# Kernel tuning notes

Measured on AMD Instinct MI355X. Metric: run time of the kernel, lower is better.

## Reference

```python
import jax, jax.numpy as jnp
import numpy as np

N_NODES = 100000
N_EDGES = 1000000
D_IN = 64
D_HID = 64
D_OUT = 64
LL_OUT = 16
NUM_REL = 5
METAPATH = (0, 1, 2)


def setup_inputs() -> dict:
    key = jax.random.key(0)
    ks = jax.random.split(key, 12)
    s = 0.05  # small init scale
    x = jax.random.normal(ks[0], (N_NODES, D_IN), dtype=jnp.float32)
    edge_index = jax.random.randint(ks[1], (2, N_EDGES), 0, N_NODES, dtype=jnp.int64)
    edge_type = jax.random.randint(ks[2], (N_EDGES,), 0, NUM_REL, dtype=jnp.int64)
    # conv1: per-relation weights + root weight + bias (input_dim -> hidden_dim)
    W1 = jax.random.normal(ks[3], (NUM_REL, D_IN, D_HID), dtype=jnp.float32) * s
    root1 = jax.random.normal(ks[4], (D_IN, D_HID), dtype=jnp.float32) * s
    b1 = jnp.zeros((D_HID,), dtype=jnp.float32)
    # conv2: hidden_dim -> output_dim (reused for all layers > 0)
    W2 = jax.random.normal(ks[5], (NUM_REL, D_HID, D_OUT), dtype=jnp.float32) * s
    root2 = jax.random.normal(ks[6], (D_HID, D_OUT), dtype=jnp.float32) * s
    b2 = jnp.zeros((D_OUT,), dtype=jnp.float32)
    # final linear layer (output_dim -> ll_output_dim)
    Wl = jax.random.normal(ks[7], (D_OUT, LL_OUT), dtype=jnp.float32) * s
    bl = jnp.zeros((LL_OUT,), dtype=jnp.float32)
    return {
        "x": x, "edge_index": edge_index, "edge_type": edge_type,
        "W1": W1, "root1": root1, "b1": b1,
        "W2": W2, "root2": root2, "b2": b2,
        "Wl": Wl, "bl": bl,
    }


def _rgcn_single_rel(rel, x, src, dst, edge_type, W, root, b):
    """RGCN conv restricted to one relation `rel`.

    flow='target_to_source': messages are gathered from the target node
    (edge_index[1]) and aggregated (sum) at the source node (edge_index[0]).
    Edges of other relation types are masked out (jit-friendly equivalent
    of boolean edge filtering).
    """
    mask = (edge_type == rel).astype(x.dtype)[:, None]          # [E, 1]
    msg = (x[dst] * mask) @ W[rel]                              # [E, d_out]
    agg = jax.ops.segment_sum(msg, src, num_segments=N_NODES)   # [N, d_out]
    return agg + x @ root + b


def reference(x, edge_index, edge_type, W1, root1, b1, W2, root2, b2, Wl, bl):
    src, dst = edge_index[0], edge_index[1]
    for layer_index, rel in enumerate(METAPATH):
        if layer_index == 0:
            x = jax.nn.relu(_rgcn_single_rel(rel, x, src, dst, edge_type, W1, root1, b1))
        else:
            x = jax.nn.relu(_rgcn_single_rel(rel, x, src, dst, edge_type, W2, root2, b2))
    logits = x @ Wl + bl
    return jax.nn.log_softmax(logits, axis=1)
```

## Files before the change

### kernel.cpp

```cpp
#include <hip/hip_runtime.h>
#include <hip/hip_bf16.h>
#include <math.h>

#define N_NODES 100000
#define N_EDGES 1000000
#define D 64
#define N3 300000
#define BCAP 16
#define BM 128
#define AST 72
#define BST 72
#define GEMM_BLOCKS ((N_NODES + BM - 1) / BM)
#define FILL_BLOCKS ((N_EDGES + 1023) / 1024)

typedef __attribute__((ext_vector_type(8))) short bf16x8;
typedef __attribute__((ext_vector_type(4))) float f32x4;

static __device__ __forceinline__ float bf2f(unsigned short u) {
    union { unsigned int i; float f; } c; c.i = ((unsigned int)u) << 16; return c.f;
}
static __device__ __forceinline__ float lo16(unsigned int u) { return bf2f((unsigned short)(u & 0xffffu)); }
static __device__ __forceinline__ float hi16(unsigned int u) { return bf2f((unsigned short)(u >> 16)); }
static __device__ __forceinline__ unsigned short f2bf(float f) {
    union { float f; unsigned int i; } c; c.f = f;
    unsigned int i = c.i;
    return (unsigned short)((i + 0x7FFFu + ((i >> 16) & 1u)) >> 16);
}
static __device__ __forceinline__ unsigned int pk2(float lo, float hi) {
    return (unsigned int)f2bf(lo) | ((unsigned int)f2bf(hi) << 16);
}

static __device__ __forceinline__ void fill_body4(
    const int* __restrict__ src, const int* __restrict__ dst,
    const int* __restrict__ et, int* __restrict__ cnt, int* __restrict__ bucket,
    int e0)
{
    if (e0 >= N_EDGES) return;
    int4 t4 = *(const int4*)(et + e0);
    int4 s4 = *(const int4*)(src + e0);
    int4 d4 = *(const int4*)(dst + e0);
    int t[4] = { t4.x, t4.y, t4.z, t4.w };
    int s[4] = { s4.x, s4.y, s4.z, s4.w };
    int d[4] = { d4.x, d4.y, d4.z, d4.w };
#pragma unroll
    for (int i = 0; i < 4; ++i) {
        if (t[i] < 3) {
            int base = t[i] * N_NODES + s[i];
            int pos = atomicAdd(&cnt[base], 1);
            if (pos < BCAP) bucket[(size_t)base * BCAP + pos] = d[i];
        }
    }
}

static __device__ __forceinline__ void gemm_body(
    int bid,
    const float* __restrict__ Hin, const unsigned short* __restrict__ Pp,
    const unsigned short* __restrict__ Yp,
    const int* __restrict__ cnt, const int* __restrict__ bucket, int relG,
    const float* __restrict__ Wm, const float* __restrict__ Rm,
    const float* __restrict__ bias,
    unsigned short* __restrict__ Y16, unsigned short* __restrict__ P16, int nN)
{
    __shared__ unsigned short At[BM][AST];
    __shared__ unsigned short Bt[128][BST];
    int t = threadIdx.x;
    int n0 = bid * BM;

#pragma unroll
    for (int it = 0; it < 8; ++it) {
        int idx = t + it * 256;
        int col = idx & 127;
        int k0  = (idx >> 7) * 4;
        const float* srcB = (col < 64) ? (Wm + col) : (Rm + col - 64);
        ushort4 wv;
        wv.x = f2bf(srcB[(k0 + 0) * 64]);
        wv.y = f2bf(srcB[(k0 + 1) * 64]);
        wv.z = f2bf(srcB[(k0 + 2) * 64]);
        wv.w = f2bf(srcB[(k0 + 3) * 64]);
        *(ushort4*)&Bt[col][k0] = wv;
    }

    {
        int gidx = t >> 4, j = t & 15, lane = t & 63, grp = lane & 48;
        if (relG < 0) {
#pragma unroll
            for (int pass = 0; pass < 8; ++pass) {
                int rw = gidx + pass * 16;
                int node = n0 + rw;
                float4 v = make_float4(0.f, 0.f, 0.f, 0.f);
                if (node < nN) v = *(const float4*)(Hin + (size_t)node * 64 + j * 4);
                ushort4 av;
                av.x = f2bf(v.x); av.y = f2bf(v.y); av.z = f2bf(v.z); av.w = f2bf(v.w);
                *(ushort4*)&At[rw][j * 4] = av;
            }
        } else {
            int nn[8]; int bk[8]; ushort4 pv[8];
#pragma unroll
            for (int p = 0; p < 8; ++p) {
                int node = n0 + gidx + p * 16;
                int nodeC = (node < nN) ? node : 0;
                int base = relG * N_NODES + nodeC;
                nn[p] = cnt[base];
                bk[p] = bucket[(size_t)base * BCAP + j];
                pv[p] = *(const ushort4*)(Pp + (size_t)nodeC * 64 + j * 4);
            }
#pragma unroll
            for (int p = 0; p < 8; ++p) {
                int rw = gidx + p * 16;
                int node = n0 + rw;
                float4 v = make_float4(0.f, 0.f, 0.f, 0.f);
                if (node < nN) {
                    v = make_float4(bf2f(pv[p].x), bf2f(pv[p].y),
                                    bf2f(pv[p].z), bf2f(pv[p].w));
                    int n = nn[p]; if (n > BCAP) n = BCAP;
                    for (int k = 0; k < n; k += 4) {
                        int i1 = (k + 1 < n) ? k + 1 : k;
                        int i2 = (k + 2 < n) ? k + 2 : k;
                        int i3 = (k + 3 < n) ? k + 3 : k;
                        int dn0 = __shfl(bk[p], grp | k);
                        int dn1 = __shfl(bk[p], grp | i1);
                        int dn2 = __shfl(bk[p], grp | i2);
                        int dn3 = __shfl(bk[p], grp | i3);
                        ushort4 u0 = *(const ushort4*)(Yp + (size_t)dn0 * 64 + j * 4);
                        ushort4 u1 = *(const ushort4*)(Yp + (size_t)dn1 * 64 + j * 4);
                        ushort4 u2 = *(const ushort4*)(Yp + (size_t)dn2 * 64 + j * 4);
                        ushort4 u3 = *(const ushort4*)(Yp + (size_t)dn3 * 64 + j * 4);
                        v.x += bf2f(u0.x); v.y += bf2f(u0.y);
                        v.z += bf2f(u0.z); v.w += bf2f(u0.w);
                        if (k + 1 < n) {
                            v.x += bf2f(u1.x); v.y += bf2f(u1.y);
                            v.z += bf2f(u1.z); v.w += bf2f(u1.w);
                        }
                        if (k + 2 < n) {
                            v.x += bf2f(u2.x); v.y += bf2f(u2.y);
                            v.z += bf2f(u2.z); v.w += bf2f(u2.w);
                        }
                        if (k + 3 < n) {
                            v.x += bf2f(u3.x); v.y += bf2f(u3.y);
                            v.z += bf2f(u3.z); v.w += bf2f(u3.w);
                        }
                    }
                    v.x = fmaxf(v.x, 0.f); v.y = fmaxf(v.y, 0.f);
                    v.z = fmaxf(v.z, 0.f); v.w = fmaxf(v.w, 0.f);
                }
                ushort4 av;
                av.x = f2bf(v.x); av.y = f2bf(v.y); av.z = f2bf(v.z); av.w = f2bf(v.w);
                *(ushort4*)&At[rw][j * 4] = av;
            }
        }
    }
    __syncthreads();

    int w  = t >> 6;
    int l  = t & 63;
    int ln = l & 15;
    int lk = l >> 4;
    f32x4 acc[2][8];
#pragma unroll
    for (int nt = 0; nt < 2; ++nt)
#pragma unroll
        for (int ct = 0; ct < 8; ++ct)
            acc[nt][ct] = (f32x4){0.f, 0.f, 0.f, 0.f};

    bf16x8 af[2][2];
#pragma unroll
    for (int nt = 0; nt < 2; ++nt)
#pragma unroll
        for (int ks = 0; ks < 2; ++ks)
            af[nt][ks] = *(const bf16x8*)&At[w * 32 + nt * 16 + ln][ks * 32 + lk * 8];

#pragma unroll
    for (int ct = 0; ct < 8; ++ct) {
        bf16x8 bf0 = *(const bf16x8*)&Bt[ct * 16 + ln][lk * 8];
        bf16x8 bf1 = *(const bf16x8*)&Bt[ct * 16 + ln][32 + lk * 8];
#pragma unroll
        for (int nt = 0; nt < 2; ++nt) {
            acc[nt][ct] = __builtin_amdgcn_mfma_f32_16x16x32_bf16(bf0, af[nt][0], acc[nt][ct], 0, 0, 0);
            acc[nt][ct] = __builtin_amdgcn_mfma_f32_16x16x32_bf16(bf1, af[nt][1], acc[nt][ct], 0, 0, 0);
        }
    }

#pragma unroll
    for (int ct = 0; ct < 8; ++ct) {
        int c0 = ct * 16 + lk * 4;
#pragma unroll
        for (int nt = 0; nt < 2; ++nt) {
            int node = n0 + w * 32 + nt * 16 + ln;
            if (node >= nN) continue;
            f32x4 v = acc[nt][ct];
            if (ct < 4) {
                uint2 u;
                u.x = pk2(v[0], v[1]);
                u.y = pk2(v[2], v[3]);
                *(uint2*)(Y16 + (size_t)node * 64 + c0) = u;
            } else {
                const float4 bv = *(const float4*)(bias + (c0 - 64));
                uint2 u;
                u.x = pk2(v[0] + bv.x, v[1] + bv.y);
                u.y = pk2(v[2] + bv.z, v[3] + bv.w);
                *(uint2*)(P16 + (size_t)node * 64 + (c0 - 64)) = u;
            }
        }
    }
}

__global__ __launch_bounds__(256) void fused0_kernel(
    const float* __restrict__ x,
    const int* __restrict__ src, const int* __restrict__ dst,
    const int* __restrict__ et, int* __restrict__ cnt, int* __restrict__ bucket,
    const float* __restrict__ Wm, const float* __restrict__ Rm,
    const float* __restrict__ bias,
    unsigned short* __restrict__ Y16, unsigned short* __restrict__ P16, int nN)
{
    if (blockIdx.x < GEMM_BLOCKS) {
        gemm_body(blockIdx.x, x, nullptr, nullptr, nullptr, nullptr, -1,
                  Wm, Rm, bias, Y16, P16, nN);
    } else {
        int e0 = ((blockIdx.x - GEMM_BLOCKS) * 256 + threadIdx.x) * 4;
        fill_body4(src, dst, et, cnt, bucket, e0);
    }
}

__global__ __launch_bounds__(256) void gemm_node_kernel(
    const unsigned short* __restrict__ Pp, const unsigned short* __restrict__ Yp,
    const int* __restrict__ cnt, const int* __restrict__ bucket, int rel,
    const float* __restrict__ Wm, const float* __restrict__ Rm,
    const float* __restrict__ bias,
    unsigned short* __restrict__ Y16, unsigned short* __restrict__ P16, int nN)
{
    gemm_body(blockIdx.x, nullptr, Pp, Yp, cnt, bucket, rel,
              Wm, Rm, bias, Y16, P16, nN);
}

__global__ __launch_bounds__(256) void final_kernel(
    const unsigned short* __restrict__ P2, const unsigned short* __restrict__ Y2,
    const int* __restrict__ cnt, const int* __restrict__ bucket, int rel,
    const float* __restrict__ Wl, const float* __restrict__ bl,
    float* __restrict__ out, int nN)
{
    int t = threadIdx.x;
    int w = t >> 6, l = t & 63;
    int ln = l & 15, lk = l >> 4;
    int node = blockIdx.x * 64 + w * 16 + ln;

    bf16x8 wf[2];
#pragma unroll
    for (int ks = 0; ks < 2; ++ks) {
        union { bf16x8 v; unsigned short u[8]; } tmp;
#pragma unroll
        for (int i = 0; i < 8; ++i)
            tmp.u[i] = f2bf(Wl[(ks * 32 + lk * 8 + i) * 16 + ln]);
        wf[ks] = tmp.v;
    }

    float v[16];
#pragma unroll
    for (int i = 0; i < 16; ++i) v[i] = 0.f;
    if (node < nN) {
#pragma unroll
        for (int ks = 0; ks < 2; ++ks) {
            uint4 pu = *(const uint4*)(P2 + (size_t)node * 64 + ks * 32 + lk * 8);
            v[ks * 8 + 0] = lo16(pu.x); v[ks * 8 + 1] = hi16(pu.x);
            v[ks * 8 + 2] = lo16(pu.y); v[ks * 8 + 3] = hi16(pu.y);
            v[ks * 8 + 4] = lo16(pu.z); v[ks * 8 + 5] = hi16(pu.z);
            v[ks * 8 + 6] = lo16(pu.w); v[ks * 8 + 7] = hi16(pu.w);
        }
        int base = rel * N_NODES + node;
        int n = cnt[base]; if (n > BCAP) n = BCAP;
        const int* brow = bucket + (size_t)base * BCAP;
        for (int k = 0; k < n; k += 2) {
            int dn0 = brow[k];
            int dn1 = (k + 1 < n) ? brow[k + 1] : dn0;
            uint4 a0 = *(const uint4*)(Y2 + (size_t)dn0 * 64 + lk * 8);
            uint4 a1 = *(const uint4*)(Y2 + (size_t)dn0 * 64 + 32 + lk * 8);
            uint4 b0 = *(const uint4*)(Y2 + (size_t)dn1 * 64 + lk * 8);
            uint4 b1 = *(const uint4*)(Y2 + (size_t)dn1 * 64 + 32 + lk * 8);
            v[0] += lo16(a0.x); v[1] += hi16(a0.x);
            v[2] += lo16(a0.y); v[3] += hi16(a0.y);
            v[4] += lo16(a0.z); v[5] += hi16(a0.z);
            v[6] += lo16(a0.w); v[7] += hi16(a0.w);
            v[8]  += lo16(a1.x); v[9]  += hi16(a1.x);
            v[10] += lo16(a1.y); v[11] += hi16(a1.y);
            v[12] += lo16(a1.z); v[13] += hi16(a1.z);
            v[14] += lo16(a1.w); v[15] += hi16(a1.w);
            if (k + 1 < n) {
                v[0] += lo16(b0.x); v[1] += hi16(b0.x);
                v[2] += lo16(b0.y); v[3] += hi16(b0.y);
                v[4] += lo16(b0.z); v[5] += hi16(b0.z);
                v[6] += lo16(b0.w); v[7] += hi16(b0.w);
                v[8]  += lo16(b1.x); v[9]  += hi16(b1.x);
                v[10] += lo16(b1.y); v[11] += hi16(b1.y);
                v[12] += lo16(b1.z); v[13] += hi16(b1.z);
                v[14] += lo16(b1.w); v[15] += hi16(b1.w);
            }
        }
#pragma unroll
        for (int i = 0; i < 16; ++i) v[i] = fmaxf(v[i], 0.f);
    }
    union { bf16x8 bv; unsigned short u[8]; } af[2];
#pragma unroll
    for (int ks = 0; ks < 2; ++ks)
#pragma unroll
        for (int i = 0; i < 8; ++i) af[ks].u[i] = f2bf(v[ks * 8 + i]);

    f32x4 acc = (f32x4){0.f, 0.f, 0.f, 0.f};
    acc = __builtin_amdgcn_mfma_f32_16x16x32_bf16(wf[0], af[0].bv, acc, 0, 0, 0);
    acc = __builtin_amdgcn_mfma_f32_16x16x32_bf16(wf[1], af[1].bv, acc, 0, 0, 0);

    if (node < nN) {
        float4 blv = *(const float4*)(bl + lk * 4);
        float p0 = acc[0] + blv.x, p1 = acc[1] + blv.y;
        float p2 = acc[2] + blv.z, p3 = acc[3] + blv.w;
        float mx = fmaxf(fmaxf(p0, p1), fmaxf(p2, p3));
        mx = fmaxf(mx, __shfl_xor(mx, 16));
        mx = fmaxf(mx, __shfl_xor(mx, 32));
        float s = __expf(p0 - mx) + __expf(p1 - mx) + __expf(p2 - mx) + __expf(p3 - mx);
        s += __shfl_xor(s, 16);
        s += __shfl_xor(s, 32);
        float ls = logf(s) + mx;
        float4 r = make_float4(p0 - ls, p1 - ls, p2 - ls, p3 - ls);
        *(float4*)(out + (size_t)node * 16 + lk * 4) = r;
    }
}

extern "C" void kernel_launch(void* const* d_in, const int* in_sizes, int n_in,
                              void* d_out, int out_size, void* d_ws, size_t ws_size,
                              hipStream_t stream) {
    const float* x     = (const float*)d_in[0];
    const int*   ei    = (const int*)  d_in[1];
    const int*   et    = (const int*)  d_in[2];
    const float* W1    = (const float*)d_in[3];
    const float* root1 = (const float*)d_in[4];
    const float* b1    = (const float*)d_in[5];
    const float* W2    = (const float*)d_in[6];
    const float* root2 = (const float*)d_in[7];
    const float* b2    = (const float*)d_in[8];
    const float* Wl    = (const float*)d_in[9];
    const float* bl    = (const float*)d_in[10];
    float* out = (float*)d_out;

    const int N = N_NODES, E = N_EDGES;
    const size_t hBytes   = (size_t)N * D * sizeof(unsigned short);
    const size_t cntBytes = ((size_t)N3 * sizeof(int) + 255) & ~(size_t)255;
    const size_t bktBytes = ((size_t)N3 * BCAP * sizeof(int) + 255) & ~(size_t)255;

    char* ws = (char*)d_ws;
    unsigned short* Ya = (unsigned short*)ws;                 ws += hBytes;
    unsigned short* Yb = (unsigned short*)ws;                 ws += hBytes;
    unsigned short* Pa = (unsigned short*)ws;                 ws += hBytes;
    unsigned short* Pb = (unsigned short*)ws;                 ws += hBytes;
    int* cnt    = (int*)ws;                                   ws += cntBytes;
    int* bucket = (int*)ws;                                   ws += bktBytes;

    const int* src = ei;
    const int* dst = ei + E;

    const int finalBlocks = (N + 63) / 64;

    hipMemsetAsync(cnt, 0, (size_t)N3 * sizeof(int), stream);

    fused0_kernel<<<GEMM_BLOCKS + FILL_BLOCKS, 256, 0, stream>>>(
        x, src, dst, et, cnt, bucket, W1 + 0 * D * D, root1, b1, Ya, Pa, N);

    gemm_node_kernel<<<GEMM_BLOCKS, 256, 0, stream>>>(
        Pa, Ya, cnt, bucket, 0, W2 + 1 * D * D, root2, b2, Yb, Pb, N);

    gemm_node_kernel<<<GEMM_BLOCKS, 256, 0, stream>>>(
        Pb, Yb, cnt, bucket, 1, W2 + 2 * D * D, root2, b2, Ya, Pa, N);

    final_kernel<<<finalBlocks, 256, 0, stream>>>(
        Pa, Ya, cnt, bucket, 2, Wl, bl, out, N);
}
```

Measured before the change: 108.5 us.

## Split per-relation bucket fill across layer kernels to overlap with GEMMs

The edge bucketing for relations 1 and 2 is no longer done entirely in the first fused kernel. Each kernel now fills only the relation needed by the next layer, in extra blocks that run alongside the current layer's GEMM blocks. This spreads the atomic-heavy fill work across three launches so it can overlap with compute instead of all sitting in the first launch. In exchange, the edge arrays are read three times instead of once, and each later kernel gets more blocks.

```diff
diff --git a/kernel.cpp b/kernel.cpp
--- a/kernel.cpp
+++ b/kernel.cpp
@@ -33,7 +33,7 @@
 static __device__ __forceinline__ void fill_body4(
     const int* __restrict__ src, const int* __restrict__ dst,
     const int* __restrict__ et, int* __restrict__ cnt, int* __restrict__ bucket,
-    int e0)
+    int e0, int rel)
 {
     if (e0 >= N_EDGES) return;
     int4 t4 = *(const int4*)(et + e0);
@@ -44,8 +44,8 @@
     int d[4] = { d4.x, d4.y, d4.z, d4.w };
 #pragma unroll
     for (int i = 0; i < 4; ++i) {
-        if (t[i] < 3) {
-            int base = t[i] * N_NODES + s[i];
+        if (t[i] == rel) {
+            int base = rel * N_NODES + s[i];
             int pos = atomicAdd(&cnt[base], 1);
             if (pos < BCAP) bucket[(size_t)base * BCAP + pos] = d[i];
         }
@@ -217,19 +217,26 @@
                   Wm, Rm, bias, Y16, P16, nN);
     } else {
         int e0 = ((blockIdx.x - GEMM_BLOCKS) * 256 + threadIdx.x) * 4;
-        fill_body4(src, dst, et, cnt, bucket, e0);
-    }
-}
-
-__global__ __launch_bounds__(256) void gemm_node_kernel(
+        fill_body4(src, dst, et, cnt, bucket, e0, 0);
+    }
+}
+
+__global__ __launch_bounds__(256) void gemm_fill_kernel(
     const unsigned short* __restrict__ Pp, const unsigned short* __restrict__ Yp,
-    const int* __restrict__ cnt, const int* __restrict__ bucket, int rel,
+    const int* __restrict__ src, const int* __restrict__ dst,
+    const int* __restrict__ et, int* __restrict__ cnt, int* __restrict__ bucket,
+    int relG, int relF,
     const float* __restrict__ Wm, const float* __restrict__ Rm,
     const float* __restrict__ bias,
     unsigned short* __restrict__ Y16, unsigned short* __restrict__ P16, int nN)
 {
-    gemm_body(blockIdx.x, nullptr, Pp, Yp, cnt, bucket, rel,
-              Wm, Rm, bias, Y16, P16, nN);
+    if (blockIdx.x < GEMM_BLOCKS) {
+        gemm_body(blockIdx.x, nullptr, Pp, Yp, cnt, bucket, relG,
+                  Wm, Rm, bias, Y16, P16, nN);
+    } else {
+        int e0 = ((blockIdx.x - GEMM_BLOCKS) * 256 + threadIdx.x) * 4;
+        fill_body4(src, dst, et, cnt, bucket, e0, relF);
+    }
 }
 
 __global__ __launch_bounds__(256) void final_kernel(
@@ -356,17 +363,20 @@
     const int* dst = ei + E;
 
     const int finalBlocks = (N + 63) / 64;
+    const int fusedBlocks = GEMM_BLOCKS + FILL_BLOCKS;
 
     hipMemsetAsync(cnt, 0, (size_t)N3 * sizeof(int), stream);
 
-    fused0_kernel<<<GEMM_BLOCKS + FILL_BLOCKS, 256, 0, stream>>>(
+    fused0_kernel<<<fusedBlocks, 256, 0, stream>>>(
         x, src, dst, et, cnt, bucket, W1 + 0 * D * D, root1, b1, Ya, Pa, N);
 
-    gemm_node_kernel<<<GEMM_BLOCKS, 256, 0, stream>>>(
-        Pa, Ya, cnt, bucket, 0, W2 + 1 * D * D, root2, b2, Yb, Pb, N);
-
-    gemm_node_kernel<<<GEMM_BLOCKS, 256, 0, stream>>>(
-        Pb, Yb, cnt, bucket, 1, W2 + 2 * D * D, root2, b2, Ya, Pa, N);
+    gemm_fill_kernel<<<fusedBlocks, 256, 0, stream>>>(
+        Pa, Ya, src, dst, et, cnt, bucket, 0, 1,
+        W2 + 1 * D * D, root2, b2, Yb, Pb, N);
+
+    gemm_fill_kernel<<<fusedBlocks, 256, 0, stream>>>(
+        Pb, Yb, src, dst, et, cnt, bucket, 1, 2,
+        W2 + 2 * D * D, root2, b2, Ya, Pa, N);
 
     final_kernel<<<finalBlocks, 256, 0, stream>>>(
         Pa, Ya, cnt, bucket, 2, Wl, bl, out, N);
```

Result: faster. 95.29 us (-12.2%).
